# Kernel optimization log

Hardware: AMD Instinct MI355X
Metric: run time of the kernel (lower is better)

Reference implementation:

```python
import jax, jax.numpy as jnp
import numpy as np

DIM = 768
HEADS = 12
HEAD_DIM = DIM // HEADS
B, N = 8, 1024


def setup_inputs() -> dict:
    key = jax.random.key(0)
    ks = jax.random.split(key, 5)
    x = jax.random.normal(ks[0], (B, N, DIM), dtype=jnp.float32)
    shared_rel_pos = jax.random.normal(ks[1], (HEADS, N, N), dtype=jnp.float32)
    qkv_w = jax.random.normal(ks[2], (3 * DIM, DIM), dtype=jnp.float32) * (DIM ** -0.5)
    proj_w = jax.random.normal(ks[3], (DIM, DIM), dtype=jnp.float32) * (DIM ** -0.5)
    proj_b = jnp.zeros((DIM,), dtype=jnp.float32)
    return {"x": x, "shared_rel_pos": shared_rel_pos, "qkv_w": qkv_w,
            "proj_w": proj_w, "proj_b": proj_b}


def reference(x, shared_rel_pos, qkv_w, proj_w, proj_b):
    Bt, Nt, C = x.shape
    scale = HEAD_DIM ** -0.5
    # qkv: Linear(dim, 3*dim, bias=False) -> (B, N, 3, H, hd) -> (3, B, H, N, hd)
    qkv = jnp.einsum('bnc,oc->bno', x, qkv_w)
    qkv = qkv.reshape(Bt, Nt, 3, HEADS, HEAD_DIM).transpose(2, 0, 3, 1, 4)
    q, k, v = qkv[0], qkv[1], qkv[2]
    # scaled dot-product attention with shared relative-position bias
    attn = jnp.einsum('bhqd,bhkd->bhqk', q, k) * scale
    attn = attn + shared_rel_pos[None]  # broadcast over batch
    attn = jax.nn.softmax(attn, axis=-1)
    out = jnp.einsum('bhqk,bhkd->bhqd', attn, v)
    out = out.transpose(0, 2, 1, 3).reshape(Bt, Nt, C)
    return jnp.einsum('bnc,oc->bno', out, proj_w) + proj_b
```

## Files before the change

### kernel.cpp

```cpp
#include <hip/hip_runtime.h>
#include <hip/hip_bf16.h>
#include <stdint.h>

#define HEADS 12
#define HD 64
#define SEQ 1024
#define CDIM 768
#define LOG2E 1.44269504f

typedef __attribute__((ext_vector_type(8))) short bfrag;
typedef __attribute__((ext_vector_type(4))) float facc;
typedef __attribute__((ext_vector_type(4))) _Float16 h4;
typedef __attribute__((ext_vector_type(2))) __fp16 pk2;

__device__ __forceinline__ ushort f2bf(float f) {
    union { float f; uint32_t u; } v; v.f = f;
    uint32_t u = v.u;
    uint32_t r = (u + 0x7FFFu + ((u >> 16) & 1u)) >> 16;
    return (ushort)r;
}
__device__ __forceinline__ ushort f2h(float f) {
    union { _Float16 h; ushort u; } c; c.h = (_Float16)f; return c.u;
}
__device__ __forceinline__ float h2f(uint32_t u16) {
    union { _Float16 h; ushort u; } c; c.u = (ushort)u16; return (float)c.h;
}
__device__ __forceinline__ h4 pack4h(float p0, float p1, float p2, float p3) {
    union { h4 v4; pk2 v2[2]; } u;
    u.v2[0] = __builtin_amdgcn_cvt_pkrtz(p0, p1);
    u.v2[1] = __builtin_amdgcn_cvt_pkrtz(p2, p3);
    return u.v4;
}

__global__ void cvt_all(const float* __restrict__ x, const float* __restrict__ qw,
                        const float* __restrict__ pw,
                        ushort* __restrict__ xd, ushort* __restrict__ qd,
                        ushort* __restrict__ pd) {
    long i = ((long)blockIdx.x * 256 + threadIdx.x) * 4;
    if (i < 6291456) {
        float4 v = *(const float4*)(x + i);
        ushort4 o = {f2bf(v.x), f2bf(v.y), f2bf(v.z), f2bf(v.w)};
        *(ushort4*)(xd + i) = o;
    } else if (i < 8060928) {
        long j = i - 6291456;
        float4 v = *(const float4*)(qw + j);
        ushort4 o = {f2bf(v.x), f2bf(v.y), f2bf(v.z), f2bf(v.w)};
        *(ushort4*)(qd + j) = o;
    } else if (i < 8650752) {
        long j = i - 8060928;
        float4 v = *(const float4*)(pw + j);
        ushort4 o = {f2bf(v.x), f2bf(v.y), f2bf(v.z), f2bf(v.w)};
        *(ushort4*)(pd + j) = o;
    }
}

#define GLOAD16(gsrc, ldst) \
    __builtin_amdgcn_global_load_lds((const __attribute__((address_space(1))) uint32_t*)(gsrc), \
                                     (__attribute__((address_space(3))) uint32_t*)(ldst), 16, 0, 0)

template<int EPI>
__global__ __launch_bounds__(256) void gemm_nt(
    const ushort* __restrict__ A, const ushort* __restrict__ Bm,
    ushort* __restrict__ qb, ushort* __restrict__ kb, ushort* __restrict__ vb,
    const float* __restrict__ projb, float* __restrict__ out,
    const float* __restrict__ relf, ushort* __restrict__ biash)
{
    __shared__ ushort As[128 * 32];
    __shared__ ushort Bs[128 * 32];
    const int t = threadIdx.x;

    if (EPI == 0 && blockIdx.y >= 18) {
        long cb = (long)(blockIdx.y - 18) * 64 + blockIdx.x;
        long i = (cb * 256 + t) * 4;
        if (i < 12582912) {
            float4 v = *(const float4*)(relf + i);
            ushort4 o = {f2h(v.x * LOG2E), f2h(v.y * LOG2E),
                         f2h(v.z * LOG2E), f2h(v.w * LOG2E)};
            *(ushort4*)(biash + i) = o;
        }
        return;
    }

    const int w = t >> 6, l = t & 63;
    const int wm = w >> 1, wn = w & 1;
    const int lr = l & 15, lg = l >> 4;
    const int m0 = blockIdx.x * 128;
    const int o0 = blockIdx.y * 128;

    facc acc[4][4] = {};

    const int srow = w * 16 + (l >> 2);
    const int scol = (l & 3) * 8;
    const ushort* Ag = A + (size_t)(m0 + srow) * CDIM + scol;
    const ushort* Bg = Bm + (size_t)(o0 + srow) * CDIM + scol;

    for (int k0 = 0; k0 < CDIM; k0 += 32) {
        __syncthreads();
        GLOAD16(Ag + k0,             As + w * 512);
        GLOAD16(Ag + 64 * CDIM + k0, As + 2048 + w * 512);
        GLOAD16(Bg + k0,             Bs + w * 512);
        GLOAD16(Bg + 64 * CDIM + k0, Bs + 2048 + w * 512);
        __syncthreads();
        bfrag af[4], bf[4];
#pragma unroll
        for (int m = 0; m < 4; ++m)
            af[m] = *(const bfrag*)&As[(wm * 64 + m * 16 + lr) * 32 + lg * 8];
#pragma unroll
        for (int n = 0; n < 4; ++n)
            bf[n] = *(const bfrag*)&Bs[(wn * 64 + n * 16 + lr) * 32 + lg * 8];
#pragma unroll
        for (int m = 0; m < 4; ++m)
#pragma unroll
            for (int n = 0; n < 4; ++n)
                acc[m][n] = __builtin_amdgcn_mfma_f32_16x16x32_bf16(af[m], bf[n], acc[m][n], 0, 0, 0);
    }

    if (EPI == 0) {
        const int tsel = o0 / CDIM;
        const int h_base = (o0 % CDIM) / 64;
        ushort* dst = (tsel == 0) ? qb : ((tsel == 1) ? kb : vb);
        const float scl = (tsel == 0) ? 0.18033688f : 1.0f;
#pragma unroll
        for (int m = 0; m < 4; ++m) {
            int grow = m0 + wm * 64 + m * 16 + lg * 4;
#pragma unroll
            for (int n = 0; n < 4; ++n) {
                int h = h_base + wn;
                int d = n * 16 + lr;
#pragma unroll
                for (int r = 0; r < 4; ++r) {
                    int row = grow + r;
                    int b = row >> 10, nn = row & 1023;
                    ushort val = (tsel == 2) ? f2h(acc[m][n][r])
                                             : f2bf(acc[m][n][r] * scl);
                    dst[(((size_t)(b * HEADS + h)) * SEQ + nn) * HD + d] = val;
                }
            }
        }
    } else {
#pragma unroll
        for (int m = 0; m < 4; ++m) {
            int grow = m0 + wm * 64 + m * 16 + lg * 4;
#pragma unroll
            for (int n = 0; n < 4; ++n) {
                int o = o0 + wn * 64 + n * 16 + lr;
                float bias = projb[o];
#pragma unroll
                for (int r = 0; r < 4; ++r)
                    out[(size_t)(grow + r) * CDIM + o] = acc[m][n][r] + bias;
            }
        }
    }
}

__global__ __launch_bounds__(256, 3) void attn_kernel(
    const ushort* __restrict__ qbuf, const ushort* __restrict__ kbuf,
    const ushort* __restrict__ vbuf, const ushort* __restrict__ biash,
    ushort* __restrict__ attn_out)
{
    __shared__ ushort Ks[2][64 * 72];
    __shared__ ushort Vt[2][64 * 72];

    const int t = threadIdx.x;
    const int w = t >> 6, l = t & 63;
    const int lr = l & 15, lg = l >> 4;

    const int bid = blockIdx.x;
    const int lid = (bid & 7) * 96 + (bid >> 3);
    const int h  = lid >> 6;
    const int qt = (lid >> 3) & 7;
    const int b  = lid & 7;

    const int q0 = qt * 128;
    const size_t headoff = (size_t)(b * HEADS + h) * SEQ * HD;
    const int qrb = q0 + w * 32;

    bfrag aQ[2][2];
#pragma unroll
    for (int n = 0; n < 2; ++n) {
        const ushort* Qp = qbuf + headoff + (size_t)(qrb + n * 16 + lr) * HD;
        aQ[n][0] = *(const bfrag*)(Qp + lg * 8);
        aQ[n][1] = *(const bfrag*)(Qp + 32 + lg * 8);
    }

    float mrun[2] = {-1e30f, -1e30f}, lrun[2] = {0.0f, 0.0f};
    facc Ov[2][4] = {};

    const ushort* bprow[2];
#pragma unroll
    for (int n = 0; n < 2; ++n)
        bprow[n] = biash + ((size_t)h * SEQ + qrb + n * 16 + lr) * SEQ;

    const int krow = t >> 3, kc = (t & 7) * 8;
    const int p2 = t & 31, vg_ = t >> 5;
    const ushort* kgb = kbuf + headoff + (size_t)krow * HD + kc;
    const ushort* vgb = vbuf + headoff + (size_t)(2 * p2) * HD + vg_ * 8;

    bfrag krA = *(const bfrag*)(kgb);
    bfrag krB = *(const bfrag*)(kgb + (size_t)32 * HD);
    bfrag vrA = *(const bfrag*)(vgb);
    bfrag vrB = *(const bfrag*)(vgb + HD);
    uint2 bcur[2][4];
#pragma unroll
    for (int n = 0; n < 2; ++n)
#pragma unroll
        for (int c = 0; c < 4; ++c)
            bcur[n][c] = *(const uint2*)(bprow[n] + c * 16 + lg * 4);

    *(bfrag*)&Ks[0][krow * 72 + kc] = krA;
    *(bfrag*)&Ks[0][(krow + 32) * 72 + kc] = krB;
#pragma unroll
    for (int i = 0; i < 8; ++i) {
        uint32_t pk = (uint32_t)(uint16_t)vrA[i] | ((uint32_t)(uint16_t)vrB[i] << 16);
        *(uint32_t*)&Vt[0][(vg_ * 8 + i) * 72 + 2 * p2] = pk;
    }
    krA = *(const bfrag*)(kgb + (size_t)64 * HD);
    krB = *(const bfrag*)(kgb + (size_t)96 * HD);
    vrA = *(const bfrag*)(vgb + (size_t)64 * HD);
    vrB = *(const bfrag*)(vgb + (size_t)65 * HD);
    __syncthreads();

    for (int tt = 0; tt < 16; ++tt) {
        const int cur = tt & 1;
        const ushort* Kc = Ks[cur];
        const ushort* Vc = Vt[cur];

        facc St[2][4];
        h4 pf[2][4];
        float psum[2] = {0.0f, 0.0f};
        float pmax[2] = {-3.0e38f, -3.0e38f};
#pragma unroll
        for (int c = 0; c < 4; ++c) {
            bfrag kf0 = *(const bfrag*)&Kc[(c * 16 + lr) * 72 + lg * 8];
            bfrag kf1 = *(const bfrag*)&Kc[(c * 16 + lr) * 72 + 32 + lg * 8];
#pragma unroll
            for (int n = 0; n < 2; ++n) {
                uint2 bb = bcur[n][c];
                facc s;
                s[0] = h2f(bb.x & 0xffffu);
                s[1] = h2f(bb.x >> 16);
                s[2] = h2f(bb.y & 0xffffu);
                s[3] = h2f(bb.y >> 16);
                __builtin_amdgcn_s_setprio(1);
                s = __builtin_amdgcn_mfma_f32_16x16x32_bf16(kf0, aQ[n][0], s, 0, 0, 0);
                s = __builtin_amdgcn_mfma_f32_16x16x32_bf16(kf1, aQ[n][1], s, 0, 0, 0);
                __builtin_amdgcn_s_setprio(0);
                St[n][c] = s;
                float p0 = exp2f(s[0] - mrun[n]);
                float p1 = exp2f(s[1] - mrun[n]);
                float p2f = exp2f(s[2] - mrun[n]);
                float p3 = exp2f(s[3] - mrun[n]);
                psum[n] += (p0 + p1) + (p2f + p3);
                pmax[n] = fmaxf(pmax[n], fmaxf(fmaxf(s[0], s[1]), fmaxf(s[2], s[3])));
                pf[n][c] = pack4h(p0, p1, p2f, p3);
            }
        }

        if (tt < 15) {
            const int kvn = (tt + 1) << 6;
#pragma unroll
            for (int n = 0; n < 2; ++n)
#pragma unroll
                for (int c = 0; c < 4; ++c)
                    bcur[n][c] = *(const uint2*)(bprow[n] + kvn + c * 16 + lg * 4);
        }

        int viol = (pmax[0] > mrun[0] + 14.0f) || (pmax[1] > mrun[1] + 14.0f);
        if (__any(viol)) {
#pragma unroll
            for (int n = 0; n < 2; ++n) {
                float pm = pmax[n];
                pm = fmaxf(pm, __shfl_xor(pm, 16));
                pm = fmaxf(pm, __shfl_xor(pm, 32));
                float mnew = fmaxf(mrun[n], pm);
                float al = exp2f(mrun[n] - mnew);
                psum[n] = 0.0f;
#pragma unroll
                for (int c = 0; c < 4; ++c) {
                    float p0 = exp2f(St[n][c][0] - mnew);
                    float p1 = exp2f(St[n][c][1] - mnew);
                    float p2f = exp2f(St[n][c][2] - mnew);
                    float p3 = exp2f(St[n][c][3] - mnew);
                    psum[n] += (p0 + p1) + (p2f + p3);
                    pf[n][c] = pack4h(p0, p1, p2f, p3);
                }
#pragma unroll
                for (int r = 0; r < 4; ++r) {
                    float a = __shfl(al, lg * 4 + r);
#pragma unroll
                    for (int d = 0; d < 4; ++d) Ov[n][d][r] *= a;
                }
                lrun[n] *= al;
                mrun[n] = mnew;
            }
        }
#pragma unroll
        for (int n = 0; n < 2; ++n) {
            psum[n] += __shfl_xor(psum[n], 16);
            psum[n] += __shfl_xor(psum[n], 32);
            lrun[n] += psum[n];
        }

        if (tt < 15) {
            *(bfrag*)&Ks[cur ^ 1][krow * 72 + kc] = krA;
            *(bfrag*)&Ks[cur ^ 1][(krow + 32) * 72 + kc] = krB;
#pragma unroll
            for (int i = 0; i < 8; ++i) {
                uint32_t pk = (uint32_t)(uint16_t)vrA[i] | ((uint32_t)(uint16_t)vrB[i] << 16);
                *(uint32_t*)&Vt[cur ^ 1][(vg_ * 8 + i) * 72 + 2 * p2] = pk;
            }
        }
        if (tt < 14) {
            const int kvn = (tt + 2) << 6;
            krA = *(const bfrag*)(kgb + (size_t)kvn * HD);
            krB = *(const bfrag*)(kgb + (size_t)(kvn + 32) * HD);
            vrA = *(const bfrag*)(vgb + (size_t)kvn * HD);
            vrB = *(const bfrag*)(vgb + (size_t)(kvn + 1) * HD);
        }

        __builtin_amdgcn_s_setprio(1);
#pragma unroll
        for (int d0 = 0; d0 < 4; ++d0) {
#pragma unroll
            for (int c = 0; c < 4; ++c) {
                h4 bv = *(const h4*)&Vc[(d0 * 16 + lr) * 72 + c * 16 + lg * 4];
#pragma unroll
                for (int n = 0; n < 2; ++n)
                    Ov[n][d0] = __builtin_amdgcn_mfma_f32_16x16x16f16(pf[n][c], bv, Ov[n][d0], 0, 0, 0);
            }
        }
        __builtin_amdgcn_s_setprio(0);

        if (tt < 15) __syncthreads();
    }

#pragma unroll
    for (int n = 0; n < 2; ++n) {
        ushort* op = attn_out + ((size_t)b * SEQ + qrb + n * 16) * CDIM + h * HD;
#pragma unroll
        for (int r = 0; r < 4; ++r) {
            float ll = __shfl(lrun[n], lg * 4 + r);
            float rl = 1.0f / ll;
#pragma unroll
            for (int d = 0; d < 4; ++d)
                op[(size_t)(lg * 4 + r) * CDIM + d * 16 + lr] = f2bf(Ov[n][d][r] * rl);
        }
    }
}

extern "C" void kernel_launch(void* const* d_in, const int* in_sizes, int n_in,
                              void* d_out, int out_size, void* d_ws, size_t ws_size,
                              hipStream_t stream) {
    const float* x     = (const float*)d_in[0];
    const float* rel   = (const float*)d_in[1];
    const float* qkvw  = (const float*)d_in[2];
    const float* projw = (const float*)d_in[3];
    const float* projb = (const float*)d_in[4];
    float* out = (float*)d_out;

    char* ws = (char*)d_ws;
    ushort* biash = (ushort*)(ws);
    ushort* qb    = (ushort*)(ws + 25165824);
    ushort* kb    = (ushort*)(ws + 37748736);
    ushort* vb    = (ushort*)(ws + 50331648);
    ushort* attnb = (ushort*)(ws + 62914560);
    ushort* xbf   = attnb;
    ushort* wbf   = (ushort*)(ws + 75497472);
    ushort* pwbf  = (ushort*)(ws + 79036416);

    cvt_all<<<8448, 256, 0, stream>>>(x, qkvw, projw, xbf, wbf, pwbf);

    gemm_nt<0><<<dim3(64, 210), 256, 0, stream>>>(xbf, wbf, qb, kb, vb, nullptr, nullptr, rel, biash);
    attn_kernel<<<768, 256, 0, stream>>>(qb, kb, vb, biash, attnb);
    gemm_nt<1><<<dim3(64, 6), 256, 0, stream>>>(attnb, pwbf, nullptr, nullptr, nullptr, projb, out, nullptr, nullptr);
}
```

Before: 150.6 us.

## Software-pipeline attention QK/softmax with previous tile's PV and interleave bias-convert blocks

```diff
diff --git a/kernel.cpp b/kernel.cpp
--- a/kernel.cpp
+++ b/kernel.cpp
@@ -69,23 +69,31 @@
     __shared__ ushort Bs[128 * 32];
     const int t = threadIdx.x;
 
-    if (EPI == 0 && blockIdx.y >= 18) {
-        long cb = (long)(blockIdx.y - 18) * 64 + blockIdx.x;
-        long i = (cb * 256 + t) * 4;
-        if (i < 12582912) {
-            float4 v = *(const float4*)(relf + i);
-            ushort4 o = {f2h(v.x * LOG2E), f2h(v.y * LOG2E),
-                         f2h(v.z * LOG2E), f2h(v.w * LOG2E)};
-            *(ushort4*)(biash + i) = o;
-        }
-        return;
+    int m0, o0;
+    if (EPI == 0) {
+        const int slot = blockIdx.x;
+        if (slot >= 12) {
+            long c = (long)blockIdx.y * 128 + (slot - 12);
+            long i = (c * 256 + t) * 4;
+            if (i < 12582912) {
+                float4 v = *(const float4*)(relf + i);
+                ushort4 o = {f2h(v.x * LOG2E), f2h(v.y * LOG2E),
+                             f2h(v.z * LOG2E), f2h(v.w * LOG2E)};
+                *(ushort4*)(biash + i) = o;
+            }
+            return;
+        }
+        const int g = blockIdx.y * 12 + slot;
+        m0 = (g & 63) * 128;
+        o0 = (g >> 6) * 128;
+    } else {
+        m0 = blockIdx.x * 128;
+        o0 = blockIdx.y * 128;
     }
 
     const int w = t >> 6, l = t & 63;
     const int wm = w >> 1, wn = w & 1;
     const int lr = l & 15, lg = l >> 4;
-    const int m0 = blockIdx.x * 128;
-    const int o0 = blockIdx.y * 128;
 
     facc acc[4][4] = {};
 
@@ -196,39 +204,39 @@
     const ushort* kgb = kbuf + headoff + (size_t)krow * HD + kc;
     const ushort* vgb = vbuf + headoff + (size_t)(2 * p2) * HD + vg_ * 8;
 
-    bfrag krA = *(const bfrag*)(kgb);
-    bfrag krB = *(const bfrag*)(kgb + (size_t)32 * HD);
-    bfrag vrA = *(const bfrag*)(vgb);
-    bfrag vrB = *(const bfrag*)(vgb + HD);
+    bfrag krA, krB, vrA, vrB;
     uint2 bcur[2][4];
-#pragma unroll
-    for (int n = 0; n < 2; ++n)
-#pragma unroll
-        for (int c = 0; c < 4; ++c)
-            bcur[n][c] = *(const uint2*)(bprow[n] + c * 16 + lg * 4);
-
-    *(bfrag*)&Ks[0][krow * 72 + kc] = krA;
-    *(bfrag*)&Ks[0][(krow + 32) * 72 + kc] = krB;
-#pragma unroll
-    for (int i = 0; i < 8; ++i) {
-        uint32_t pk = (uint32_t)(uint16_t)vrA[i] | ((uint32_t)(uint16_t)vrB[i] << 16);
-        *(uint32_t*)&Vt[0][(vg_ * 8 + i) * 72 + 2 * p2] = pk;
-    }
-    krA = *(const bfrag*)(kgb + (size_t)64 * HD);
-    krB = *(const bfrag*)(kgb + (size_t)96 * HD);
-    vrA = *(const bfrag*)(vgb + (size_t)64 * HD);
-    vrB = *(const bfrag*)(vgb + (size_t)65 * HD);
-    __syncthreads();
-
-    for (int tt = 0; tt < 16; ++tt) {
-        const int cur = tt & 1;
-        const ushort* Kc = Ks[cur];
-        const ushort* Vc = Vt[cur];
-
-        facc St[2][4];
-        h4 pf[2][4];
-        float psum[2] = {0.0f, 0.0f};
-        float pmax[2] = {-3.0e38f, -3.0e38f};
+    facc St[2][4];
+    h4 pfN[2][4], pfP[2][4];
+    float psum[2], pmax[2];
+
+    auto load_regs = [&](int ti) {
+        const size_t kv = (size_t)ti << 6;
+        krA = *(const bfrag*)(kgb + kv * HD);
+        krB = *(const bfrag*)(kgb + (kv + 32) * HD);
+        vrA = *(const bfrag*)(vgb + kv * HD);
+        vrB = *(const bfrag*)(vgb + (kv + 1) * HD);
+    };
+    auto load_bias = [&](int ti) {
+        const int kvn = ti << 6;
+#pragma unroll
+        for (int n = 0; n < 2; ++n)
+#pragma unroll
+            for (int c = 0; c < 4; ++c)
+                bcur[n][c] = *(const uint2*)(bprow[n] + kvn + c * 16 + lg * 4);
+    };
+    auto stage = [&](int buf) {
+        *(bfrag*)&Ks[buf][krow * 72 + kc] = krA;
+        *(bfrag*)&Ks[buf][(krow + 32) * 72 + kc] = krB;
+#pragma unroll
+        for (int i = 0; i < 8; ++i) {
+            uint32_t pk = (uint32_t)(uint16_t)vrA[i] | ((uint32_t)(uint16_t)vrB[i] << 16);
+            *(uint32_t*)&Vt[buf][(vg_ * 8 + i) * 72 + 2 * p2] = pk;
+        }
+    };
+    auto qk_exp = [&](const ushort* Kc) {
+#pragma unroll
+        for (int n = 0; n < 2; ++n) { psum[n] = 0.0f; pmax[n] = -3.0e38f; }
 #pragma unroll
         for (int c = 0; c < 4; ++c) {
             bfrag kf0 = *(const bfrag*)&Kc[(c * 16 + lr) * 72 + lg * 8];
@@ -252,19 +260,25 @@
                 float p3 = exp2f(s[3] - mrun[n]);
                 psum[n] += (p0 + p1) + (p2f + p3);
                 pmax[n] = fmaxf(pmax[n], fmaxf(fmaxf(s[0], s[1]), fmaxf(s[2], s[3])));
-                pf[n][c] = pack4h(p0, p1, p2f, p3);
-            }
-        }
-
-        if (tt < 15) {
-            const int kvn = (tt + 1) << 6;
-#pragma unroll
-            for (int n = 0; n < 2; ++n)
-#pragma unroll
-                for (int c = 0; c < 4; ++c)
-                    bcur[n][c] = *(const uint2*)(bprow[n] + kvn + c * 16 + lg * 4);
-        }
-
+                pfN[n][c] = pack4h(p0, p1, p2f, p3);
+            }
+        }
+    };
+    auto pv = [&](const ushort* Vc, const h4 (&pA)[2][4]) {
+        __builtin_amdgcn_s_setprio(1);
+#pragma unroll
+        for (int d0 = 0; d0 < 4; ++d0) {
+#pragma unroll
+            for (int c = 0; c < 4; ++c) {
+                h4 bv = *(const h4*)&Vc[(d0 * 16 + lr) * 72 + c * 16 + lg * 4];
+#pragma unroll
+                for (int n = 0; n < 2; ++n)
+                    Ov[n][d0] = __builtin_amdgcn_mfma_f32_16x16x16f16(pA[n][c], bv, Ov[n][d0], 0, 0, 0);
+            }
+        }
+        __builtin_amdgcn_s_setprio(0);
+    };
+    auto defer_lrun = [&]() {
         int viol = (pmax[0] > mrun[0] + 14.0f) || (pmax[1] > mrun[1] + 14.0f);
         if (__any(viol)) {
 #pragma unroll
@@ -282,7 +296,7 @@
                     float p2f = exp2f(St[n][c][2] - mnew);
                     float p3 = exp2f(St[n][c][3] - mnew);
                     psum[n] += (p0 + p1) + (p2f + p3);
-                    pf[n][c] = pack4h(p0, p1, p2f, p3);
+                    pfN[n][c] = pack4h(p0, p1, p2f, p3);
                 }
 #pragma unroll
                 for (int r = 0; r < 4; ++r) {
@@ -296,43 +310,43 @@
         }
 #pragma unroll
         for (int n = 0; n < 2; ++n) {
-            psum[n] += __shfl_xor(psum[n], 16);
-            psum[n] += __shfl_xor(psum[n], 32);
-            lrun[n] += psum[n];
-        }
-
-        if (tt < 15) {
-            *(bfrag*)&Ks[cur ^ 1][krow * 72 + kc] = krA;
-            *(bfrag*)&Ks[cur ^ 1][(krow + 32) * 72 + kc] = krB;
-#pragma unroll
-            for (int i = 0; i < 8; ++i) {
-                uint32_t pk = (uint32_t)(uint16_t)vrA[i] | ((uint32_t)(uint16_t)vrB[i] << 16);
-                *(uint32_t*)&Vt[cur ^ 1][(vg_ * 8 + i) * 72 + 2 * p2] = pk;
-            }
-        }
-        if (tt < 14) {
-            const int kvn = (tt + 2) << 6;
-            krA = *(const bfrag*)(kgb + (size_t)kvn * HD);
-            krB = *(const bfrag*)(kgb + (size_t)(kvn + 32) * HD);
-            vrA = *(const bfrag*)(vgb + (size_t)kvn * HD);
-            vrB = *(const bfrag*)(vgb + (size_t)(kvn + 1) * HD);
-        }
-
-        __builtin_amdgcn_s_setprio(1);
-#pragma unroll
-        for (int d0 = 0; d0 < 4; ++d0) {
-#pragma unroll
-            for (int c = 0; c < 4; ++c) {
-                h4 bv = *(const h4*)&Vc[(d0 * 16 + lr) * 72 + c * 16 + lg * 4];
-#pragma unroll
-                for (int n = 0; n < 2; ++n)
-                    Ov[n][d0] = __builtin_amdgcn_mfma_f32_16x16x16f16(pf[n][c], bv, Ov[n][d0], 0, 0, 0);
-            }
-        }
-        __builtin_amdgcn_s_setprio(0);
-
-        if (tt < 15) __syncthreads();
-    }
+            float s = psum[n];
+            s += __shfl_xor(s, 16);
+            s += __shfl_xor(s, 32);
+            lrun[n] += s;
+        }
+    };
+    auto pf_rotate = [&]() {
+#pragma unroll
+        for (int n = 0; n < 2; ++n)
+#pragma unroll
+            for (int c = 0; c < 4; ++c)
+                pfP[n][c] = pfN[n][c];
+    };
+
+    load_regs(0);
+    load_bias(0);
+    stage(0);
+    load_regs(1);
+    __syncthreads();
+    qk_exp(Ks[0]);
+    load_bias(1);
+    defer_lrun();
+    pf_rotate();
+
+    for (int tt = 0; tt < 15; ++tt) {
+        const int cur = tt & 1;
+        stage(cur ^ 1);
+        if (tt < 14) load_regs(tt + 2);
+        __syncthreads();
+        qk_exp(Ks[cur ^ 1]);
+        if (tt < 14) load_bias(tt + 2);
+        pv(Vt[cur], pfP);
+        defer_lrun();
+        pf_rotate();
+        __syncthreads();
+    }
+    pv(Vt[1], pfP);
 
 #pragma unroll
     for (int n = 0; n < 2; ++n) {
@@ -370,7 +384,7 @@
 
     cvt_all<<<8448, 256, 0, stream>>>(x, qkvw, projw, xbf, wbf, pwbf);
 
-    gemm_nt<0><<<dim3(64, 210), 256, 0, stream>>>(xbf, wbf, qb, kb, vb, nullptr, nullptr, rel, biash);
+    gemm_nt<0><<<dim3(140, 96), 256, 0, stream>>>(xbf, wbf, qb, kb, vb, nullptr, nullptr, rel, biash);
     attn_kernel<<<768, 256, 0, stream>>>(qb, kb, vb, biash, attnb);
     gemm_nt<1><<<dim3(64, 6), 256, 0, stream>>>(attnb, pwbf, nullptr, nullptr, nullptr, projb, out, nullptr, nullptr);
 }
```

Measured after the change: 157.7 us. +4.7%, slower.
